# Kernel tuning notes

Measured on AMD Instinct MI355X. Metric: run time of the kernel, lower is better.

The kernel has to match this reference:

```python
import jax, jax.numpy as jnp
import numpy as np

VOCAB = 8192
HIDDEN = 1024
BATCH = 64
SEQ = 256


def setup_inputs() -> dict:
    key = jax.random.key(0)
    k1, k2, k3, k4 = jax.random.split(key, 4)
    return {
        "X": jax.random.randint(k1, (BATCH, SEQ), 0, VOCAB, dtype=jnp.int64 if jax.config.jax_enable_x64 else jnp.int32),
        "status": jnp.zeros((BATCH, HIDDEN), dtype=jnp.float32),
        "w_xh": 0.01 * jax.random.normal(k2, (VOCAB, HIDDEN), dtype=jnp.float32),
        "w_hh": 0.01 * jax.random.normal(k3, (HIDDEN, HIDDEN), dtype=jnp.float32),
        "w_ho": 0.01 * jax.random.normal(k4, (HIDDEN, VOCAB), dtype=jnp.float32),
        "b_h": jnp.zeros((HIDDEN,), dtype=jnp.float32),
        "b_o": jnp.zeros((VOCAB,), dtype=jnp.float32),
    }


def reference(X, status, w_xh, w_hh, w_ho, b_h, b_o):
    # one_hot(X.T) @ w_xh is exactly a row gather from w_xh (same math, no
    # [S,B,V] one-hot materialized):  xs[t, b] = w_xh[X[b, t]]
    xs = w_xh[X.T]  # (S, B, H)

    def step(h, xe):
        h = jnp.tanh(h @ w_hh + xe + b_h)  # (B, H)
        y = h @ w_ho + b_o                 # (B, V)
        return h, y

    h_final, Y = jax.lax.scan(step, status, xs)
    return Y, h_final  # Y: (S, B, V) matching torch.cat over timesteps
```

## Files before the change

### kernel.cpp

```cpp
#include <hip/hip_runtime.h>
#include <hip/hip_bf16.h>
#include <stdint.h>

#define VOCAB 8192
#define HIDDEN 1024
#define BATCH 64
#define SEQ 256

#define NPROD 64
#define NCONS 192
#define GBM 128
#define GBN 128
#define GBK 32
#define NT_M ((SEQ * BATCH) / GBM)
#define NT_N (VOCAB / GBN)

typedef __attribute__((ext_vector_type(8))) short short8;
typedef __attribute__((ext_vector_type(4))) float floatx4;

__device__ __forceinline__ short f2bf(float x) {
    __hip_bfloat16 h = __float2bfloat16(x);
    return *reinterpret_cast<short*>(&h);
}

__device__ __forceinline__ void load_lds16(const void* g, void* l) {
    __builtin_amdgcn_global_load_lds(
        (const __attribute__((address_space(1))) void*)(uintptr_t)g,
        (__attribute__((address_space(3))) void*)(uint32_t)(uintptr_t)l,
        16, 0, 0);
}

__device__ __forceinline__ void st_h(short* p, short v) {
    __hip_atomic_store(p, v, __ATOMIC_RELAXED, __HIP_MEMORY_SCOPE_AGENT);
}


__global__ void cast_h0(const float* __restrict__ s, short* __restrict__ d) {
    int i = blockIdx.x * 256 + threadIdx.x;
    d[i] = f2bf(s[i]);
}

__global__ void transpose_cast(const float* __restrict__ who, short* __restrict__ whoT) {
    __shared__ float tile[32][33];
    int n0 = blockIdx.x * 32;
    int k0 = blockIdx.y * 32;
    for (int r = threadIdx.y; r < 32; r += 8)
        tile[r][threadIdx.x] = who[(size_t)(k0 + r) * VOCAB + n0 + threadIdx.x];
    __syncthreads();
    for (int r = threadIdx.y; r < 32; r += 8)
        whoT[(size_t)(n0 + r) * HIDDEN + k0 + threadIdx.x] = f2bf(tile[threadIdx.x][r]);
}

__global__ __launch_bounds__(256) void rnn_fused(
    short* __restrict__ Hall,
    const float* __restrict__ w_hh, const float* __restrict__ w_xh,
    const float* __restrict__ b_h, const int* __restrict__ X,
    float* __restrict__ hfin, int* bar, int* prog,
    const short* __restrict__ whoT, const float* __restrict__ b_o,
    float* __restrict__ C) {
    __shared__ __align__(16) short smem[16 * 1032];
    const int tid = threadIdx.x;

    if (blockIdx.x < NPROD) {
        short* Bs = smem;
        const int g = blockIdx.x;
        const int w = tid >> 6, lane = tid & 63;
        const int q = lane >> 4, r15 = lane & 15;

        for (int idx = tid; idx < 16 * 1024; idx += 256) {
            int c = idx & 15, k = idx >> 4;
            Bs[c * 1032 + k] = f2bf(w_hh[(size_t)k * HIDDEN + g * 16 + c]);
        }
        __syncthreads();

        const int jcol = g * 16 + r15;
        const float bh = b_h[jcol];
        int brow[4];
#pragma unroll
        for (int r = 0; r < 4; r++) brow[r] = w * 16 + q * 4 + r;
        const int afr_off = (w * 16 + r15) * HIDDEN + q * 8;

        int xr[4];
#pragma unroll
        for (int r = 0; r < 4; r++) xr[r] = X[brow[r] * SEQ];
        float xe[4];
#pragma unroll
        for (int r = 0; r < 4; r++) xe[r] = w_xh[(size_t)xr[r] * HIDDEN + jcol];
#pragma unroll
        for (int r = 0; r < 4; r++) xr[r] = X[brow[r] * SEQ + 1];

        for (int t = 0; t < SEQ; t++) {
            float xen[4];
            if (t + 1 < SEQ) {
#pragma unroll
                for (int r = 0; r < 4; r++) xen[r] = w_xh[(size_t)xr[r] * HIDDEN + jcol];
                if (t + 2 < SEQ) {
#pragma unroll
                    for (int r = 0; r < 4; r++) xr[r] = X[brow[r] * SEQ + t + 2];
                }
            }

            const short* Ab = Hall + (size_t)t * (BATCH * HIDDEN) + afr_off;
            floatx4 a0 = {0.f, 0.f, 0.f, 0.f}, a1 = a0, a2 = a0, a3 = a0;
#pragma unroll
            for (int k0 = 0; k0 < HIDDEN; k0 += 128) {
                short8 f0 = *(const short8*)(Ab + k0);
                short8 f1 = *(const short8*)(Ab + k0 + 32);
                short8 f2 = *(const short8*)(Ab + k0 + 64);
                short8 f3 = *(const short8*)(Ab + k0 + 96);
                const short* Bb = &Bs[r15 * 1032 + k0 + q * 8];
                short8 b0 = *(const short8*)(Bb);
                short8 b1 = *(const short8*)(Bb + 32);
                short8 b2 = *(const short8*)(Bb + 64);
                short8 b3 = *(const short8*)(Bb + 96);
                a0 = __builtin_amdgcn_mfma_f32_16x16x32_bf16(f0, b0, a0, 0, 0, 0);
                a1 = __builtin_amdgcn_mfma_f32_16x16x32_bf16(f1, b1, a1, 0, 0, 0);
                a2 = __builtin_amdgcn_mfma_f32_16x16x32_bf16(f2, b2, a2, 0, 0, 0);
                a3 = __builtin_amdgcn_mfma_f32_16x16x32_bf16(f3, b3, a3, 0, 0, 0);
            }
            floatx4 acc = (a0 + a1) + (a2 + a3);

            short* Hnext = Hall + (size_t)(t + 1) * (BATCH * HIDDEN);
#pragma unroll
            for (int r = 0; r < 4; r++) {
                float v = acc[r] + xe[r] + bh;
                float h = tanhf(v);
                st_h(&Hnext[brow[r] * HIDDEN + jcol], f2bf(h));
                if (t == SEQ - 1) hfin[brow[r] * HIDDEN + jcol] = h;
            }

            asm volatile("s_waitcnt vmcnt(0)" ::: "memory");
            __syncthreads();
            if (tid == 0) {
                __hip_atomic_fetch_add(bar, 1, __ATOMIC_RELAXED, __HIP_MEMORY_SCOPE_AGENT);
                const int target = NPROD * (t + 1);
                while (__hip_atomic_load(bar, __ATOMIC_RELAXED, __HIP_MEMORY_SCOPE_AGENT) < target)
                    __builtin_amdgcn_s_sleep(1);
                if (g == 0)
                    __hip_atomic_store(prog, target, __ATOMIC_RELAXED, __HIP_MEMORY_SCOPE_AGENT);
            }
            __syncthreads();
            __builtin_amdgcn_fence(__ATOMIC_ACQUIRE, "workgroup");
#pragma unroll
            for (int r = 0; r < 4; r++) xe[r] = xen[r];
        }
    } else {
        short* la = smem;
        short* lb = smem + GBM * GBK;
        const short* __restrict__ A = Hall + BATCH * HIDDEN;
        const int cid = (int)blockIdx.x - NPROD;
        const int wave = tid >> 6, lane = tid & 63;
        const int wm = (wave >> 1) * 64, wn = (wave & 1) * 64;
        const int q = lane >> 4, r15 = lane & 15;
        const int col_l = lane & 15, row_q = (lane >> 4) * 4;

        for (int n = cid; n < NT_M * NT_N; n += NCONS) {
            const int ti = n / NT_N, tj = n - ti * NT_N;
            const int m0 = ti * GBM, n0 = tj * GBN;

            if (tid == 0) {
                const int needed = NPROD * (2 * ti + 2);
                while (__hip_atomic_load(prog, __ATOMIC_RELAXED, __HIP_MEMORY_SCOPE_AGENT) < needed)
                    __builtin_amdgcn_s_sleep(2);
            }
            __syncthreads();
            __builtin_amdgcn_fence(__ATOMIC_ACQUIRE, "workgroup");

            floatx4 acc[4][4] = {};
            for (int k0 = 0; k0 < HIDDEN; k0 += GBK) {
#pragma unroll
                for (int i = 0; i < 2; i++) {
                    int c = wave * 128 + i * 64 + lane;
                    int row = c >> 2, s = c & 3;
                    int gq = s ^ ((row >> 1) & 3);
                    load_lds16(&A[(size_t)(m0 + row) * HIDDEN + k0 + gq * 8], &la[c * 8]);
                    load_lds16(&whoT[(size_t)(n0 + row) * HIDDEN + k0 + gq * 8], &lb[c * 8]);
                }
                __syncthreads();

                short8 af[4], bf[4];
#pragma unroll
                for (int i = 0; i < 4; i++) {
                    int ra = wm + i * 16 + r15;
                    af[i] = *(const short8*)&la[ra * GBK + (q ^ ((ra >> 1) & 3)) * 8];
                    int rb = wn + i * 16 + r15;
                    bf[i] = *(const short8*)&lb[rb * GBK + (q ^ ((rb >> 1) & 3)) * 8];
                }
#pragma unroll
                for (int i = 0; i < 4; i++)
#pragma unroll
                    for (int jj = 0; jj < 4; jj++)
                        acc[i][jj] = __builtin_amdgcn_mfma_f32_16x16x32_bf16(af[i], bf[jj], acc[i][jj], 0, 0, 0);
                __syncthreads();
            }

#pragma unroll
            for (int i = 0; i < 4; i++) {
#pragma unroll
                for (int jj = 0; jj < 4; jj++) {
                    int col = n0 + wn + jj * 16 + col_l;
                    float bb = b_o[col];
#pragma unroll
                    for (int r = 0; r < 4; r++) {
                        int row = m0 + wm + i * 16 + row_q + r;
                        __builtin_nontemporal_store(acc[i][jj][r] + bb,
                                                    &C[(size_t)row * VOCAB + col]);
                    }
                }
            }
        }
    }
}


extern "C" void kernel_launch(void* const* d_in, const int* in_sizes, int n_in,
                              void* d_out, int out_size, void* d_ws, size_t ws_size,
                              hipStream_t stream) {
    const int*   X      = (const int*)d_in[0];
    const float* status = (const float*)d_in[1];
    const float* w_xh   = (const float*)d_in[2];
    const float* w_hh   = (const float*)d_in[3];
    const float* w_ho   = (const float*)d_in[4];
    const float* b_h    = (const float*)d_in[5];
    const float* b_o    = (const float*)d_in[6];
    float* out = (float*)d_out;

    char* ws = (char*)d_ws;
    int*   bar  = (int*)ws;
    int*   prog = (int*)(ws + 128);
    short* Hall = (short*)(ws + 4096);
    short* whoT = (short*)(ws + 4096 + (size_t)(SEQ + 1) * BATCH * HIDDEN * 2);

    hipMemsetAsync(ws, 0, 256, stream);
    cast_h0<<<BATCH * HIDDEN / 256, 256, 0, stream>>>(status, Hall);
    transpose_cast<<<dim3(VOCAB / 32, HIDDEN / 32), dim3(32, 8), 0, stream>>>(w_ho, whoT);

    rnn_fused<<<NPROD + NCONS, 256, 0, stream>>>(
        Hall, w_hh, w_xh, b_h, X,
        out + (size_t)SEQ * BATCH * VOCAB,
        bar, prog, whoT, b_o, out);
}
```

Baseline: 2.430 ms.

## Replace atomic counter barrier with per-block progress slots and fast tanh

Swaps the single fetch-add counter barrier among producer blocks for per-block progress flags in padded slots. A full wavefront polls all 64 slots at once and waits until every one has reached the step, and consumers poll the same slots instead of a separate progress word. This is meant to remove contention on one atomic and the extra hop through a designated block. Also replaces tanhf with an exp/reciprocal approximation to shorten the serial recurrence step, which may slightly reduce accuracy or overflow for large inputs.

```diff
diff --git a/kernel.cpp b/kernel.cpp
--- a/kernel.cpp
+++ b/kernel.cpp
@@ -15,6 +15,8 @@
 #define NT_M ((SEQ * BATCH) / GBM)
 #define NT_N (VOCAB / GBN)
 
+#define SLOT_STRIDE 32
+
 typedef __attribute__((ext_vector_type(8))) short short8;
 typedef __attribute__((ext_vector_type(4))) float floatx4;
 
@@ -32,6 +34,17 @@
 
 __device__ __forceinline__ void st_h(short* p, short v) {
     __hip_atomic_store(p, v, __ATOMIC_RELAXED, __HIP_MEMORY_SCOPE_AGENT);
+}
+__device__ __forceinline__ void st_slot(int* p, int v) {
+    __hip_atomic_store(p, v, __ATOMIC_RELAXED, __HIP_MEMORY_SCOPE_AGENT);
+}
+__device__ __forceinline__ int ld_slot(const int* p) {
+    return __hip_atomic_load(p, __ATOMIC_RELAXED, __HIP_MEMORY_SCOPE_AGENT);
+}
+
+__device__ __forceinline__ float fast_tanh(float x) {
+    float e2 = __expf(2.0f * x);
+    return 1.0f - 2.0f * __builtin_amdgcn_rcpf(e2 + 1.0f);
 }
 
 
@@ -55,16 +68,16 @@
     short* __restrict__ Hall,
     const float* __restrict__ w_hh, const float* __restrict__ w_xh,
     const float* __restrict__ b_h, const int* __restrict__ X,
-    float* __restrict__ hfin, int* bar, int* prog,
+    float* __restrict__ hfin, int* slots,
     const short* __restrict__ whoT, const float* __restrict__ b_o,
     float* __restrict__ C) {
     __shared__ __align__(16) short smem[16 * 1032];
     const int tid = threadIdx.x;
+    const int w = tid >> 6, lane = tid & 63;
 
     if (blockIdx.x < NPROD) {
         short* Bs = smem;
         const int g = blockIdx.x;
-        const int w = tid >> 6, lane = tid & 63;
         const int q = lane >> 4, r15 = lane & 15;
 
         for (int idx = tid; idx < 16 * 1024; idx += 256) {
@@ -124,20 +137,20 @@
 #pragma unroll
             for (int r = 0; r < 4; r++) {
                 float v = acc[r] + xe[r] + bh;
-                float h = tanhf(v);
+                float h = fast_tanh(v);
                 st_h(&Hnext[brow[r] * HIDDEN + jcol], f2bf(h));
                 if (t == SEQ - 1) hfin[brow[r] * HIDDEN + jcol] = h;
             }
 
             asm volatile("s_waitcnt vmcnt(0)" ::: "memory");
             __syncthreads();
-            if (tid == 0) {
-                __hip_atomic_fetch_add(bar, 1, __ATOMIC_RELAXED, __HIP_MEMORY_SCOPE_AGENT);
-                const int target = NPROD * (t + 1);
-                while (__hip_atomic_load(bar, __ATOMIC_RELAXED, __HIP_MEMORY_SCOPE_AGENT) < target)
+            if (tid == 0) st_slot(&slots[g * SLOT_STRIDE], t + 1);
+            if (w == 0) {
+                for (;;) {
+                    int v = ld_slot(&slots[lane * SLOT_STRIDE]);
+                    if (__all(v >= t + 1)) break;
                     __builtin_amdgcn_s_sleep(1);
-                if (g == 0)
-                    __hip_atomic_store(prog, target, __ATOMIC_RELAXED, __HIP_MEMORY_SCOPE_AGENT);
+                }
             }
             __syncthreads();
             __builtin_amdgcn_fence(__ATOMIC_ACQUIRE, "workgroup");
@@ -149,7 +162,7 @@
         short* lb = smem + GBM * GBK;
         const short* __restrict__ A = Hall + BATCH * HIDDEN;
         const int cid = (int)blockIdx.x - NPROD;
-        const int wave = tid >> 6, lane = tid & 63;
+        const int wave = w;
         const int wm = (wave >> 1) * 64, wn = (wave & 1) * 64;
         const int q = lane >> 4, r15 = lane & 15;
         const int col_l = lane & 15, row_q = (lane >> 4) * 4;
@@ -158,10 +171,13 @@
             const int ti = n / NT_N, tj = n - ti * NT_N;
             const int m0 = ti * GBM, n0 = tj * GBN;
 
-            if (tid == 0) {
-                const int needed = NPROD * (2 * ti + 2);
-                while (__hip_atomic_load(prog, __ATOMIC_RELAXED, __HIP_MEMORY_SCOPE_AGENT) < needed)
-                    __builtin_amdgcn_s_sleep(2);
+            const int needed = 2 * ti + 2;
+            if (wave == 0) {
+                for (;;) {
+                    int v = ld_slot(&slots[lane * SLOT_STRIDE]);
+                    if (__all(v >= needed)) break;
+                    __builtin_amdgcn_s_sleep(16);
+                }
             }
             __syncthreads();
             __builtin_amdgcn_fence(__ATOMIC_ACQUIRE, "workgroup");
@@ -226,17 +242,16 @@
     float* out = (float*)d_out;
 
     char* ws = (char*)d_ws;
-    int*   bar  = (int*)ws;
-    int*   prog = (int*)(ws + 128);
-    short* Hall = (short*)(ws + 4096);
-    short* whoT = (short*)(ws + 4096 + (size_t)(SEQ + 1) * BATCH * HIDDEN * 2);
-
-    hipMemsetAsync(ws, 0, 256, stream);
+    int*   slots = (int*)(ws + 512);
+    short* Hall  = (short*)(ws + 16384);
+    short* whoT  = (short*)(ws + 16384 + (size_t)(SEQ + 1) * BATCH * HIDDEN * 2);
+
+    hipMemsetAsync(ws, 0, 16384, stream);
     cast_h0<<<BATCH * HIDDEN / 256, 256, 0, stream>>>(status, Hall);
     transpose_cast<<<dim3(VOCAB / 32, HIDDEN / 32), dim3(32, 8), 0, stream>>>(w_ho, whoT);
 
     rnn_fused<<<NPROD + NCONS, 256, 0, stream>>>(
         Hall, w_hh, w_xh, b_h, X,
         out + (size_t)SEQ * BATCH * VOCAB,
-        bar, prog, whoT, b_o, out);
-}
+        slots, whoT, b_o, out);
+}
```

Measured after the change: 2.030 ms. -16.5%, faster.
